# Performance work log

Hardware: AMD Instinct MI355X
Metric: run time of the kernel (lower is better)

## Reference

```python
import jax, jax.numpy as jnp
import numpy as np

N_NODES = 20000
N_EDGES = 320000
N_GRAPHS = 128
IN_CH = 64
DIM = 32
NEG_SLOPE = 0.2
EPS = 1e-16


def _gat_conv(x, src, dst, W, att_src, att_dst, bias, heads, ch):
    """PyG GATConv (concat=True, self-loops already included in src/dst).
    x: [N, F_in]; W: [heads*ch, F_in]; att_*: [heads, ch]; bias: [heads*ch].
    Returns [N, heads*ch]."""
    N = x.shape[0]
    h = (x @ W.T).reshape(N, heads, ch)                      # [N, H, C]
    a_src = (h * att_src[None]).sum(-1)                      # [N, H]
    a_dst = (h * att_dst[None]).sum(-1)                      # [N, H]
    e = jax.nn.leaky_relu(a_src[src] + a_dst[dst], NEG_SLOPE)  # [E, H]
    # segment softmax over edges sharing a destination node
    m = jax.ops.segment_max(e, dst, num_segments=N)          # [N, H]
    ex = jnp.exp(e - m[dst])
    s = jax.ops.segment_sum(ex, dst, num_segments=N)
    alpha = ex / (s[dst] + EPS)                              # [E, H]
    msg = alpha[:, :, None] * h[src]                         # [E, H, C]
    out = jax.ops.segment_sum(msg, dst, num_segments=N)      # [N, H, C]
    return out.reshape(N, heads * ch) + bias[None, :]


def setup_inputs() -> dict:
    key = jax.random.key(0)
    ks = jax.random.split(key, 20)

    x = jax.random.normal(ks[0], (N_NODES, IN_CH), dtype=jnp.float32)
    edge_index = jax.random.randint(ks[1], (2, N_EDGES), 0, N_NODES, dtype=jnp.int64)
    batch = jnp.sort(jax.random.randint(ks[2], (N_NODES,), 0, N_GRAPHS, dtype=jnp.int64))

    def lin_init(k, shape, fan_in):
        return jax.random.normal(k, shape, dtype=jnp.float32) * (1.0 / np.sqrt(fan_in))

    H1, C1 = 5, DIM * 2      # conv1: in -> dim*2, heads 5 -> out dim*10
    H2, C2 = 5, DIM * 3      # conv2: dim*10 -> dim*3, heads 5 -> out dim*15
    H3, C3 = 1, DIM          # conv3: dim*15 -> dim, heads 1

    inp = {
        "x": x,
        "W1": lin_init(ks[3], (H1 * C1, IN_CH), IN_CH),
        "att_src1": lin_init(ks[4], (H1, C1), C1),
        "att_dst1": lin_init(ks[5], (H1, C1), C1),
        "b1": jnp.zeros((H1 * C1,), jnp.float32),
        "W2": lin_init(ks[6], (H2 * C2, H1 * C1), H1 * C1),
        "att_src2": lin_init(ks[7], (H2, C2), C2),
        "att_dst2": lin_init(ks[8], (H2, C2), C2),
        "b2": jnp.zeros((H2 * C2,), jnp.float32),
        "W3": lin_init(ks[9], (H3 * C3, H2 * C2), H2 * C2),
        "att_src3": lin_init(ks[10], (H3, C3), C3),
        "att_dst3": lin_init(ks[11], (H3, C3), C3),
        "b3": jnp.zeros((H3 * C3,), jnp.float32),
        "lin_w": lin_init(ks[12], (1024, DIM), DIM),
        "lin_b": jnp.zeros((1024,), jnp.float32),
        "lin2_w": lin_init(ks[13], (1, 1024), 1024),
        "lin2_b": jnp.zeros((1,), jnp.float32),
        "edge_index": edge_index,
        "batch": batch,
    }
    return inp


def reference(x, W1, att_src1, att_dst1, b1,
              W2, att_src2, att_dst2, b2,
              W3, att_src3, att_dst3, b3,
              lin_w, lin_b, lin2_w, lin2_b,
              edge_index, batch):
    N = x.shape[0]
    # PyG GATConv adds self-loops by default
    loops = jnp.arange(N, dtype=edge_index.dtype)
    src = jnp.concatenate([edge_index[0], loops])
    dst = jnp.concatenate([edge_index[1], loops])

    h = _gat_conv(x, src, dst, W1, att_src1, att_dst1, b1, 5, DIM * 2)
    h = jax.nn.relu(h)                                   # dropout p=0 -> identity
    h = _gat_conv(h, src, dst, W2, att_src2, att_dst2, b2, 5, DIM * 3)
    h = jax.nn.relu(h)
    h = _gat_conv(h, src, dst, W3, att_src3, att_dst3, b3, 1, DIM)
    h = jax.nn.relu(h)

    g = jax.ops.segment_sum(h, batch, num_segments=N_GRAPHS)   # global_add_pool [G, dim]
    g = jax.nn.relu(g @ lin_w.T + lin_b[None, :])
    g = g @ lin2_w.T + lin2_b[None, :]
    return jax.nn.sigmoid(g)                                   # [G, out_channels]
```

## Files before the change

kernel.cpp:

```cpp
#include <hip/hip_runtime.h>
#include <math.h>

#define NN 20000
#define NE 320000
#define NG 128

typedef short short8 __attribute__((ext_vector_type(8)));
typedef float f32x4 __attribute__((ext_vector_type(4)));
typedef float f32x2 __attribute__((ext_vector_type(2)));
typedef unsigned short ushort;
typedef unsigned short ushort4v __attribute__((ext_vector_type(4)));
typedef float float4v __attribute__((ext_vector_type(4)));
typedef unsigned int uint;
typedef unsigned int uint2v __attribute__((ext_vector_type(2)));

__device__ __forceinline__ float b2f(ushort u) {
    unsigned int v = ((unsigned int)u) << 16;
    return __uint_as_float(v);
}
__device__ __forceinline__ ushort f2b(float f) {
    unsigned int u = __float_as_uint(f);
    u = (u + 0x7fff + ((u >> 16) & 1)) >> 16;
    return (ushort)u;
}
__device__ __forceinline__ float lrelu(float x) { return x >= 0.f ? x : 0.2f * x; }
__device__ __forceinline__ unsigned char f2f8(float v) {
    return (unsigned char)(__builtin_amdgcn_cvt_pk_fp8_f32(v, v, 0, false) & 0xff);
}
__device__ __forceinline__ void dec8(uint2v r, f32x2 d[4]) {
    d[0] = __builtin_amdgcn_cvt_pk_f32_fp8(r.x, false);
    d[1] = __builtin_amdgcn_cvt_pk_f32_fp8(r.x, true);
    d[2] = __builtin_amdgcn_cvt_pk_f32_fp8(r.y, false);
    d[3] = __builtin_amdgcn_cvt_pk_f32_fp8(r.y, true);
}

#define CVT_N0 (NN * 64 / 4)
#define CVT_N1 (320 * 64 / 4)
#define CVT_N2 (480 * 320 / 4)
#define CVT_N3 (32 * 480 / 4)
__global__ void f2b4_kernel(const float* __restrict__ a0, ushort* __restrict__ o0,
                            const float* __restrict__ a1, ushort* __restrict__ o1,
                            const float* __restrict__ a2, ushort* __restrict__ o2,
                            const float* __restrict__ a3, ushort* __restrict__ o3) {
    int i = blockIdx.x * blockDim.x + threadIdx.x;
    const float* src; ushort* dst; int li;
    if (i < CVT_N0) { src = a0; dst = o0; li = i; }
    else if (i < CVT_N0 + CVT_N1) { src = a1; dst = o1; li = i - CVT_N0; }
    else if (i < CVT_N0 + CVT_N1 + CVT_N2) { src = a2; dst = o2; li = i - CVT_N0 - CVT_N1; }
    else if (i < CVT_N0 + CVT_N1 + CVT_N2 + CVT_N3) { src = a3; dst = o3; li = i - CVT_N0 - CVT_N1 - CVT_N2; }
    else return;
    float4v v = *(const float4v*)(src + (size_t)li * 4);
    ushort4v r;
    r.x = f2b(v.x); r.y = f2b(v.y); r.z = f2b(v.z); r.w = f2b(v.w);
    *(ushort4v*)(dst + (size_t)li * 4) = r;
}

__global__ void count_kernel(const int* __restrict__ dst, int* __restrict__ cnt, int E) {
    int i = blockIdx.x * blockDim.x + threadIdx.x;
    if (i < E) atomicAdd(&cnt[dst[i]], 1);
}

__global__ __launch_bounds__(1024) void scan_kernel(const int* __restrict__ cnt,
                                                    int* __restrict__ row_start, int n) {
    __shared__ int sh[1024];
    int tid = threadIdx.x;
    int base = tid * 20;
    int local[20];
    int s = 0;
    #pragma unroll
    for (int k = 0; k < 20; ++k) {
        int idx = base + k;
        int v = (idx < n) ? cnt[idx] : 0;
        local[k] = s;
        s += v;
    }
    sh[tid] = s;
    __syncthreads();
    for (int off = 1; off < 1024; off <<= 1) {
        int t = (tid >= off) ? sh[tid - off] : 0;
        __syncthreads();
        sh[tid] += t;
        __syncthreads();
    }
    int pre = (tid == 0) ? 0 : sh[tid - 1];
    #pragma unroll
    for (int k = 0; k < 20; ++k) {
        int idx = base + k;
        if (idx < n) row_start[idx] = pre + local[k];
    }
    if (tid == 1023) row_start[n] = sh[1023];
}

__global__ void fill_kernel(const int* __restrict__ src, const int* __restrict__ dst,
                            const int* __restrict__ row_start, int* __restrict__ cursor,
                            int* __restrict__ csr_src, int E) {
    int i = blockIdx.x * blockDim.x + threadIdx.x;
    if (i < E) {
        int d = dst[i];
        int pos = atomicAdd(&cursor[d], 1);
        csr_src[row_start[d] + pos] = src[i];
    }
}

template <int K, int NF, int H, bool F8>
__global__ __launch_bounds__(256) void gemm_lds(const ushort* __restrict__ A,
                                                const ushort* __restrict__ B,
                                                ushort* __restrict__ C,
                                                unsigned char* __restrict__ C8,
                                                const float* __restrict__ att_src,
                                                const float* __restrict__ att_dst,
                                                float* __restrict__ a_src,
                                                float* __restrict__ a_dst,
                                                int M, int N, int gridx) {
    constexpr int BN = NF * 16;
    constexpr int KC = (K % 160 == 0) ? 160 : K;
    constexpr int NCHK = K / KC;
    constexpr int KS = KC / 32;
    __shared__ ushort Bs[BN][KC + 8];

    const int nwg = gridDim.x;
    int bid = blockIdx.x;
    {
        int q = nwg >> 3, r = nwg & 7;
        int xcd = bid & 7, idx = bid >> 3;
        bid = (xcd < r ? xcd * (q + 1) : r * (q + 1) + (xcd - r) * q) + idx;
    }
    const int by = bid / gridx;
    const int bx = bid % gridx;
    const int bn = bx * BN;

    const int tid = threadIdx.x;
    const int w = tid >> 6;
    const int lane = tid & 63;
    const int l15 = lane & 15;
    const int lhi = lane >> 4;

    const int bm = by * 64 + w * 16;
    int arow = bm + l15;
    if (arow >= M) arow = M - 1;
    const ushort* ap = A + (size_t)arow * K + lhi * 8;

    f32x4 acc[NF];
    #pragma unroll
    for (int f = 0; f < NF; ++f) acc[f] = (f32x4){0.f, 0.f, 0.f, 0.f};

    #pragma unroll
    for (int ch = 0; ch < NCHK; ++ch) {
        const int c0 = ch * KC;
        if (ch > 0) __syncthreads();
        constexpr int NCH = BN * (KC / 8);
        for (int i = tid; i < NCH; i += 256) {
            int r = i / (KC / 8), c8 = i % (KC / 8);
            short8 v = *(const short8*)(B + (size_t)(bn + r) * K + c0 + c8 * 8);
            *(short8*)(&Bs[r][c8 * 8]) = v;
        }
        __syncthreads();

        short8 a_cur = *(const short8*)(ap + c0);
        short8 b_cur[NF], b_nxt[NF];
        #pragma unroll
        for (int f = 0; f < NF; ++f)
            b_cur[f] = *(const short8*)(&Bs[f * 16 + l15][lhi * 8]);

        #pragma unroll
        for (int ks = 0; ks < KS; ++ks) {
            short8 a_nxt = a_cur;
            if (ks + 1 < KS) {
                a_nxt = *(const short8*)(ap + c0 + (ks + 1) * 32);
                #pragma unroll
                for (int f = 0; f < NF; ++f)
                    b_nxt[f] = *(const short8*)(&Bs[f * 16 + l15][(ks + 1) * 32 + lhi * 8]);
            }
            #pragma unroll
            for (int f = 0; f < NF; ++f)
                acc[f] = __builtin_amdgcn_mfma_f32_16x16x32_bf16(a_cur, b_cur[f], acc[f], 0, 0, 0);
            a_cur = a_nxt;
            #pragma unroll
            for (int f = 0; f < NF; ++f) b_cur[f] = b_nxt[f];
        }
    }

    #pragma unroll
    for (int f = 0; f < NF; ++f) {
        #pragma unroll
        for (int j = 0; j < 4; ++j) {
            int row = bm + lhi * 4 + j;
            if (row < M) {
                if (F8) C8[(size_t)row * N + bn + f * 16 + l15] = f2f8(acc[f][j]);
                else    C[(size_t)row * N + bn + f * 16 + l15] = f2b(acc[f][j]);
            }
        }
    }

    float as_v[NF], ad_v[NF];
    #pragma unroll
    for (int f = 0; f < NF; ++f) {
        as_v[f] = att_src[bx * BN + f * 16 + l15];
        ad_v[f] = att_dst[bx * BN + f * 16 + l15];
    }
    #pragma unroll
    for (int j = 0; j < 4; ++j) {
        float ps = 0.f, pd = 0.f;
        #pragma unroll
        for (int f = 0; f < NF; ++f) {
            ps += acc[f][j] * as_v[f];
            pd += acc[f][j] * ad_v[f];
        }
        #pragma unroll
        for (int off = 1; off < 16; off <<= 1) {
            ps += __shfl_xor(ps, off);
            pd += __shfl_xor(pd, off);
        }
        int row = bm + lhi * 4 + j;
        if (l15 == 0 && row < M) {
            a_src[row * H + bx] = ps;
            a_dst[row * H + bx] = pd;
        }
    }
}

template <int H, int C>
__global__ void gat_agg_f8(const unsigned char* __restrict__ h8,
                           const float* __restrict__ a_src, const float* __restrict__ a_dst,
                           const int* __restrict__ row_start, const int* __restrict__ csr_src,
                           const float* __restrict__ bias, ushort* __restrict__ out, int N) {
    constexpr int W = H * C;
    constexpr int VL = W / 8;
    int n = (blockIdx.x * blockDim.x + threadIdx.x) >> 6;
    int lane = threadIdx.x & 63;
    if (n >= N) return;
    bool act = lane < VL;
    int l = act ? lane : 0;
    int hd = (8 * l) / C;
    float adst = a_dst[n * H + hd];

    float m = lrelu(a_src[n * H + hd] + adst);
    float ssum = 1.f;
    f32x2 acc2[4];
    {
        uint2v r = *(const uint2v*)(h8 + (size_t)n * W + 8 * l);
        dec8(r, acc2);
    }

    int rs = row_start[n], re = row_start[n + 1];
    int i = rs;
    for (; i + 8 <= re; i += 8) {
        int s[8]; uint2v r[8]; float e[8];
        #pragma unroll
        for (int j = 0; j < 8; ++j) s[j] = csr_src[i + j];
        #pragma unroll
        for (int j = 0; j < 8; ++j) r[j] = *(const uint2v*)(h8 + (size_t)s[j] * W + 8 * l);
        #pragma unroll
        for (int j = 0; j < 8; ++j) e[j] = lrelu(a_src[s[j] * H + hd] + adst);
        float nm = m;
        #pragma unroll
        for (int j = 0; j < 8; ++j) nm = fmaxf(nm, e[j]);
        float scale = __expf(m - nm);
        m = nm;
        f32x2 sc = {scale, scale};
        #pragma unroll
        for (int d = 0; d < 4; ++d) acc2[d] *= sc;
        ssum *= scale;
        float wsum = 0.f;
        #pragma unroll
        for (int j = 0; j < 8; ++j) {
            float wj = __expf(e[j] - nm);
            wsum += wj;
            f32x2 dd[4];
            dec8(r[j], dd);
            f32x2 vw = {wj, wj};
            #pragma unroll
            for (int d = 0; d < 4; ++d) acc2[d] += vw * dd[d];
        }
        ssum += wsum;
    }
    for (; i + 4 <= re; i += 4) {
        int s[4]; uint2v r[4]; float e[4];
        #pragma unroll
        for (int j = 0; j < 4; ++j) s[j] = csr_src[i + j];
        #pragma unroll
        for (int j = 0; j < 4; ++j) r[j] = *(const uint2v*)(h8 + (size_t)s[j] * W + 8 * l);
        #pragma unroll
        for (int j = 0; j < 4; ++j) e[j] = lrelu(a_src[s[j] * H + hd] + adst);
        float nm = m;
        #pragma unroll
        for (int j = 0; j < 4; ++j) nm = fmaxf(nm, e[j]);
        float scale = __expf(m - nm);
        m = nm;
        f32x2 sc = {scale, scale};
        #pragma unroll
        for (int d = 0; d < 4; ++d) acc2[d] *= sc;
        ssum *= scale;
        float wsum = 0.f;
        #pragma unroll
        for (int j = 0; j < 4; ++j) {
            float wj = __expf(e[j] - nm);
            wsum += wj;
            f32x2 dd[4];
            dec8(r[j], dd);
            f32x2 vw = {wj, wj};
            #pragma unroll
            for (int d = 0; d < 4; ++d) acc2[d] += vw * dd[d];
        }
        ssum += wsum;
    }
    for (; i < re; ++i) {
        int s = csr_src[i];
        uint2v r = *(const uint2v*)(h8 + (size_t)s * W + 8 * l);
        float e = lrelu(a_src[s * H + hd] + adst);
        float nm = fmaxf(m, e);
        float scale = __expf(m - nm);
        m = nm;
        float wgt = __expf(e - nm);
        ssum = ssum * scale + wgt;
        f32x2 dd[4];
        dec8(r, dd);
        f32x2 sc = {scale, scale};
        f32x2 vw = {wgt, wgt};
        #pragma unroll
        for (int d = 0; d < 4; ++d) acc2[d] = acc2[d] * sc + vw * dd[d];
    }

    float inv = 1.f / (ssum + 1e-16f);
    if (act) {
        short8 o;
        #pragma unroll
        for (int d = 0; d < 4; ++d) {
            #pragma unroll
            for (int e2 = 0; e2 < 2; ++e2) {
                float v = acc2[d][e2] * inv + bias[8 * l + 2 * d + e2];
                o[2 * d + e2] = (short)f2b(v > 0.f ? v : 0.f);
            }
        }
        *(short8*)(out + (size_t)n * W + 8 * l) = o;
    }
}

__global__ void gat_agg_c32(const ushort* __restrict__ h, const float* __restrict__ a_src,
                            const float* __restrict__ a_dst, const int* __restrict__ row_start,
                            const int* __restrict__ csr_src, const float* __restrict__ bias,
                            ushort* __restrict__ out, int N) {
    int n = (blockIdx.x * blockDim.x + threadIdx.x) >> 6;
    int lane = threadIdx.x & 63;
    if (n >= N) return;
    int g = lane >> 2;
    int q = lane & 3;
    float adst = a_dst[n];
    int rs = row_start[n];
    int total = row_start[n + 1] - rs + 1;

    float m = -1e30f, ssum = 0.f;
    float acc[8];
    #pragma unroll
    for (int j = 0; j < 8; ++j) acc[j] = 0.f;

    for (int k = g; k < total; k += 16) {
        int s = (k == 0) ? n : csr_src[rs + k - 1];
        float e = lrelu(a_src[s] + adst);
        float nm = fmaxf(m, e);
        float scale = __expf(m - nm);
        m = nm;
        float w = __expf(e - nm);
        ssum = ssum * scale + w;
        short8 r = *(const short8*)(h + (size_t)s * 32 + 8 * q);
        #pragma unroll
        for (int j = 0; j < 8; ++j) acc[j] = acc[j] * scale + w * b2f((ushort)r[j]);
    }

    #pragma unroll
    for (int off = 4; off < 64; off <<= 1) {
        float m2 = __shfl_xor(m, off);
        float s2 = __shfl_xor(ssum, off);
        float nm = fmaxf(m, m2);
        float sc1 = __expf(m - nm), sc2 = __expf(m2 - nm);
        ssum = ssum * sc1 + s2 * sc2;
        #pragma unroll
        for (int j = 0; j < 8; ++j) {
            float a2 = __shfl_xor(acc[j], off);
            acc[j] = acc[j] * sc1 + a2 * sc2;
        }
        m = nm;
    }

    if (lane < 4) {
        float inv = 1.f / (ssum + 1e-16f);
        short8 o;
        #pragma unroll
        for (int j = 0; j < 8; ++j) {
            float v = acc[j] * inv + bias[8 * lane + j];
            o[j] = (short)f2b(v > 0.f ? v : 0.f);
        }
        *(short8*)(out + (size_t)n * 32 + 8 * lane) = o;
    }
}

__global__ __launch_bounds__(256) void pool_graph(const ushort* __restrict__ x,
                                                  const int* __restrict__ batch,
                                                  float* __restrict__ g, int N) {
    int gr = blockIdx.x;
    int a = 0, b = N;
    while (a < b) { int mid = (a + b) >> 1; if (batch[mid] < gr) a = mid + 1; else b = mid; }
    int lo = a;
    b = N;
    while (a < b) { int mid = (a + b) >> 1; if (batch[mid] < gr + 1) a = mid + 1; else b = mid; }
    int hi = a;

    int tid = threadIdx.x;
    int c = tid & 31;
    int grp = tid >> 5;
    float s = 0.f;
    for (int n = lo + grp; n < hi; n += 8)
        s += b2f(x[(size_t)n * 32 + c]);
    __shared__ float sh[8][33];
    sh[grp][c] = s;
    __syncthreads();
    if (tid < 32) {
        float t = 0.f;
        #pragma unroll
        for (int k = 0; k < 8; ++k) t += sh[k][c];
        g[gr * 32 + c] = t;
    }
}

__global__ __launch_bounds__(256) void mlp_fused(const float* __restrict__ gpool,
                                                 const float* __restrict__ lin_w,
                                                 const float* __restrict__ lin_b,
                                                 const float* __restrict__ lin2_w,
                                                 const float* __restrict__ lin2_b,
                                                 float* __restrict__ outp) {
    int gr = blockIdx.x;
    int tid = threadIdx.x;
    __shared__ float grow[32];
    __shared__ float red[4];
    if (tid < 8) {
        float4v v = *(const float4v*)(gpool + gr * 32 + tid * 4);
        *(float4v*)(&grow[tid * 4]) = v;
    }
    __syncthreads();
    float partial = 0.f;
    #pragma unroll
    for (int u = 0; u < 4; ++u) {
        int o = tid + u * 256;
        float s = lin_b[o];
        const float* wp = lin_w + (size_t)o * 32;
        #pragma unroll
        for (int k = 0; k < 32; ++k) s += grow[k] * wp[k];
        s = s > 0.f ? s : 0.f;
        partial += s * lin2_w[o];
    }
    #pragma unroll
    for (int off = 32; off; off >>= 1) partial += __shfl_down(partial, off);
    int lane = tid & 63, wv = tid >> 6;
    if (lane == 0) red[wv] = partial;
    __syncthreads();
    if (tid == 0) {
        float t = red[0] + red[1] + red[2] + red[3] + lin2_b[0];
        outp[gr] = 1.f / (1.f + expf(-t));
    }
}

static inline size_t al256(size_t x) { return (x + 255) & ~(size_t)255; }

extern "C" void kernel_launch(void* const* d_in, const int* in_sizes, int n_in,
                              void* d_out, int out_size, void* d_ws, size_t ws_size,
                              hipStream_t stream) {
    const float* x      = (const float*)d_in[0];
    const float* W1     = (const float*)d_in[1];
    const float* as1    = (const float*)d_in[2];
    const float* ad1    = (const float*)d_in[3];
    const float* b1     = (const float*)d_in[4];
    const float* W2     = (const float*)d_in[5];
    const float* as2    = (const float*)d_in[6];
    const float* ad2    = (const float*)d_in[7];
    const float* b2     = (const float*)d_in[8];
    const float* W3     = (const float*)d_in[9];
    const float* as3    = (const float*)d_in[10];
    const float* ad3    = (const float*)d_in[11];
    const float* b3     = (const float*)d_in[12];
    const float* lin_w  = (const float*)d_in[13];
    const float* lin_b  = (const float*)d_in[14];
    const float* lin2_w = (const float*)d_in[15];
    const float* lin2_b = (const float*)d_in[16];
    const int*   ei     = (const int*)d_in[17];
    const int*   batch  = (const int*)d_in[18];
    float* outp = (float*)d_out;

    const int E = in_sizes[17] / 2;
    const int* e_src = ei;
    const int* e_dst = ei + E;

    char* p = (char*)d_ws;
    ushort* h_bf   = (ushort*)p; p += al256((size_t)NN * 480 * 2);
    ushort* o_bf   = (ushort*)p; p += al256((size_t)NN * 480 * 2);
    unsigned char* h_f8 = (unsigned char*)p; p += al256((size_t)NN * 480);
    ushort* x_bf   = (ushort*)p; p += al256((size_t)NN * 64 * 2);
    ushort* w1_bf  = (ushort*)p; p += al256((size_t)320 * 64 * 2);
    ushort* w2_bf  = (ushort*)p; p += al256((size_t)480 * 320 * 2);
    ushort* w3_bf  = (ushort*)p; p += al256((size_t)32 * 480 * 2);
    float* asrc    = (float*)p; p += al256((size_t)NN * 5 * 4);
    float* adst    = (float*)p; p += al256((size_t)NN * 5 * 4);
    int*   row_st  = (int*)p;   p += al256((size_t)(NN + 1) * 4);
    int*   cnt     = (int*)p;   p += (size_t)NN * 4;
    int*   cursor  = (int*)p;   p += (size_t)NN * 4;
    p = (char*)al256((size_t)p);
    int*   csr_src = (int*)p;   p += al256((size_t)NE * 4);
    float* gpool   = (float*)p; p += al256((size_t)NG * 32 * 4);
    (void)ws_size; (void)n_in; (void)out_size;

    dim3 blk(256);

    hipMemsetAsync(cnt, 0, (size_t)2 * NN * 4, stream);
    count_kernel<<<(E + 255) / 256, 256, 0, stream>>>(e_dst, cnt, E);
    scan_kernel<<<1, 1024, 0, stream>>>(cnt, row_st, NN);
    fill_kernel<<<(E + 255) / 256, 256, 0, stream>>>(e_src, e_dst, row_st, cursor, csr_src, E);

    {
        int tot = CVT_N0 + CVT_N1 + CVT_N2 + CVT_N3;
        f2b4_kernel<<<(tot + 255) / 256, blk, 0, stream>>>(x, x_bf, W1, w1_bf, W2, w2_bf, W3, w3_bf);
    }

    const int MPAN = (NN + 63) / 64;
    const int NBLK = (NN + 3) / 4;
    {
        gemm_lds<64, 4, 5, true><<<5 * MPAN, blk, 0, stream>>>(x_bf, w1_bf, h_bf, h_f8, as1, ad1, asrc, adst, NN, 320, 5);
        gat_agg_f8<5, 64><<<NBLK, blk, 0, stream>>>(h_f8, asrc, adst, row_st, csr_src, b1, o_bf, NN);
    }
    {
        gemm_lds<320, 6, 5, true><<<5 * MPAN, blk, 0, stream>>>(o_bf, w2_bf, h_bf, h_f8, as2, ad2, asrc, adst, NN, 480, 5);
        gat_agg_f8<5, 96><<<NBLK, blk, 0, stream>>>(h_f8, asrc, adst, row_st, csr_src, b2, o_bf, NN);
    }
    {
        gemm_lds<480, 2, 1, false><<<1 * MPAN, blk, 0, stream>>>(o_bf, w3_bf, h_bf, h_f8, as3, ad3, asrc, adst, NN, 32, 1);
        gat_agg_c32<<<NBLK, blk, 0, stream>>>(h_bf, asrc, adst, row_st, csr_src, b3, o_bf, NN);
    }
    pool_graph<<<NG, blk, 0, stream>>>(o_bf, batch, gpool, NN);
    mlp_fused<<<NG, blk, 0, stream>>>(gpool, lin_w, lin_b, lin2_w, lin2_b, outp);
}
```

Measured before the change: 194.2 us.

## Reorder GAT aggregation to head-major thread mapping and fuse small kernels

The fp8 GAT aggregation now assigns one thread per (head, node, 8-column chunk) in head-major order, with an XCD-aware block remap. Previously a 64-lane wave served each node and idle lanes were masked. The 4-edge unrolled loop is dropped. The count and bf16-conversion kernels are merged into one launch, as are pooling and the MLP, to cut launch overhead. Neighbouring threads now handle different nodes, so within a wave the gathers for a given source row become scattered, and per-head a_src lookups repeat across threads.

```diff
diff --git a/kernel.cpp b/kernel.cpp
--- a/kernel.cpp
+++ b/kernel.cpp
@@ -38,26 +38,24 @@
 #define CVT_N1 (320 * 64 / 4)
 #define CVT_N2 (480 * 320 / 4)
 #define CVT_N3 (32 * 480 / 4)
-__global__ void f2b4_kernel(const float* __restrict__ a0, ushort* __restrict__ o0,
-                            const float* __restrict__ a1, ushort* __restrict__ o1,
-                            const float* __restrict__ a2, ushort* __restrict__ o2,
-                            const float* __restrict__ a3, ushort* __restrict__ o3) {
+#define CVT_TOT (CVT_N0 + CVT_N1 + CVT_N2 + CVT_N3)
+__global__ void cvt_count_kernel(const float* __restrict__ a0, ushort* __restrict__ o0,
+                                 const float* __restrict__ a1, ushort* __restrict__ o1,
+                                 const float* __restrict__ a2, ushort* __restrict__ o2,
+                                 const float* __restrict__ a3, ushort* __restrict__ o3,
+                                 const int* __restrict__ e_dst, int* __restrict__ cnt, int E) {
     int i = blockIdx.x * blockDim.x + threadIdx.x;
+    if (i < E) atomicAdd(&cnt[e_dst[i]], 1);
     const float* src; ushort* dst; int li;
     if (i < CVT_N0) { src = a0; dst = o0; li = i; }
     else if (i < CVT_N0 + CVT_N1) { src = a1; dst = o1; li = i - CVT_N0; }
     else if (i < CVT_N0 + CVT_N1 + CVT_N2) { src = a2; dst = o2; li = i - CVT_N0 - CVT_N1; }
-    else if (i < CVT_N0 + CVT_N1 + CVT_N2 + CVT_N3) { src = a3; dst = o3; li = i - CVT_N0 - CVT_N1 - CVT_N2; }
+    else if (i < CVT_TOT) { src = a3; dst = o3; li = i - CVT_N0 - CVT_N1 - CVT_N2; }
     else return;
     float4v v = *(const float4v*)(src + (size_t)li * 4);
     ushort4v r;
     r.x = f2b(v.x); r.y = f2b(v.y); r.z = f2b(v.z); r.w = f2b(v.w);
     *(ushort4v*)(dst + (size_t)li * 4) = r;
-}
-
-__global__ void count_kernel(const int* __restrict__ dst, int* __restrict__ cnt, int E) {
-    int i = blockIdx.x * blockDim.x + threadIdx.x;
-    if (i < E) atomicAdd(&cnt[dst[i]], 1);
 }
 
 __global__ __launch_bounds__(1024) void scan_kernel(const int* __restrict__ cnt,
@@ -220,25 +218,33 @@
 }
 
 template <int H, int C>
-__global__ void gat_agg_f8(const unsigned char* __restrict__ h8,
-                           const float* __restrict__ a_src, const float* __restrict__ a_dst,
-                           const int* __restrict__ row_start, const int* __restrict__ csr_src,
-                           const float* __restrict__ bias, ushort* __restrict__ out, int N) {
+__global__ void gat_agg_f8_hm(const unsigned char* __restrict__ h8,
+                              const float* __restrict__ a_src, const float* __restrict__ a_dst,
+                              const int* __restrict__ row_start, const int* __restrict__ csr_src,
+                              const float* __restrict__ bias, ushort* __restrict__ out, int N) {
     constexpr int W = H * C;
-    constexpr int VL = W / 8;
-    int n = (blockIdx.x * blockDim.x + threadIdx.x) >> 6;
-    int lane = threadIdx.x & 63;
-    if (n >= N) return;
-    bool act = lane < VL;
-    int l = act ? lane : 0;
-    int hd = (8 * l) / C;
+    constexpr int CH = C / 8;
+    const int nwg = gridDim.x;
+    int bid = blockIdx.x;
+    {
+        int q = nwg >> 3, r = nwg & 7;
+        int xcd = bid & 7, idx = bid >> 3;
+        bid = (xcd < r ? xcd * (q + 1) : r * (q + 1) + (xcd - r) * q) + idx;
+    }
+    int t = bid * 256 + (int)threadIdx.x;
+    int hd = t / (N * CH);
+    if (hd >= H) return;
+    int rem = t - hd * (N * CH);
+    int n = rem / CH;
+    int ck = rem - n * CH;
+    int col = hd * CH + ck;
     float adst = a_dst[n * H + hd];
 
     float m = lrelu(a_src[n * H + hd] + adst);
     float ssum = 1.f;
     f32x2 acc2[4];
     {
-        uint2v r = *(const uint2v*)(h8 + (size_t)n * W + 8 * l);
+        uint2v r = *(const uint2v*)(h8 + (size_t)n * W + 8 * col);
         dec8(r, acc2);
     }
 
@@ -249,7 +255,7 @@
         #pragma unroll
         for (int j = 0; j < 8; ++j) s[j] = csr_src[i + j];
         #pragma unroll
-        for (int j = 0; j < 8; ++j) r[j] = *(const uint2v*)(h8 + (size_t)s[j] * W + 8 * l);
+        for (int j = 0; j < 8; ++j) r[j] = *(const uint2v*)(h8 + (size_t)s[j] * W + 8 * col);
         #pragma unroll
         for (int j = 0; j < 8; ++j) e[j] = lrelu(a_src[s[j] * H + hd] + adst);
         float nm = m;
@@ -274,39 +280,9 @@
         }
         ssum += wsum;
     }
-    for (; i + 4 <= re; i += 4) {
-        int s[4]; uint2v r[4]; float e[4];
-        #pragma unroll
-        for (int j = 0; j < 4; ++j) s[j] = csr_src[i + j];
-        #pragma unroll
-        for (int j = 0; j < 4; ++j) r[j] = *(const uint2v*)(h8 + (size_t)s[j] * W + 8 * l);
-        #pragma unroll
-        for (int j = 0; j < 4; ++j) e[j] = lrelu(a_src[s[j] * H + hd] + adst);
-        float nm = m;
-        #pragma unroll
-        for (int j = 0; j < 4; ++j) nm = fmaxf(nm, e[j]);
-        float scale = __expf(m - nm);
-        m = nm;
-        f32x2 sc = {scale, scale};
-        #pragma unroll
-        for (int d = 0; d < 4; ++d) acc2[d] *= sc;
-        ssum *= scale;
-        float wsum = 0.f;
-        #pragma unroll
-        for (int j = 0; j < 4; ++j) {
-            float wj = __expf(e[j] - nm);
-            wsum += wj;
-            f32x2 dd[4];
-            dec8(r[j], dd);
-            f32x2 vw = {wj, wj};
-            #pragma unroll
-            for (int d = 0; d < 4; ++d) acc2[d] += vw * dd[d];
-        }
-        ssum += wsum;
-    }
     for (; i < re; ++i) {
         int s = csr_src[i];
-        uint2v r = *(const uint2v*)(h8 + (size_t)s * W + 8 * l);
+        uint2v r = *(const uint2v*)(h8 + (size_t)s * W + 8 * col);
         float e = lrelu(a_src[s * H + hd] + adst);
         float nm = fmaxf(m, e);
         float scale = __expf(m - nm);
@@ -322,18 +298,16 @@
     }
 
     float inv = 1.f / (ssum + 1e-16f);
-    if (act) {
-        short8 o;
-        #pragma unroll
-        for (int d = 0; d < 4; ++d) {
-            #pragma unroll
-            for (int e2 = 0; e2 < 2; ++e2) {
-                float v = acc2[d][e2] * inv + bias[8 * l + 2 * d + e2];
-                o[2 * d + e2] = (short)f2b(v > 0.f ? v : 0.f);
-            }
-        }
-        *(short8*)(out + (size_t)n * W + 8 * l) = o;
-    }
+    short8 o;
+    #pragma unroll
+    for (int d = 0; d < 4; ++d) {
+        #pragma unroll
+        for (int e2 = 0; e2 < 2; ++e2) {
+            float v = acc2[d][e2] * inv + bias[8 * col + 2 * d + e2];
+            o[2 * d + e2] = (short)f2b(v > 0.f ? v : 0.f);
+        }
+    }
+    *(short8*)(out + (size_t)n * W + 8 * col) = o;
 }
 
 __global__ void gat_agg_c32(const ushort* __restrict__ h, const float* __restrict__ a_src,
@@ -394,9 +368,13 @@
     }
 }
 
-__global__ __launch_bounds__(256) void pool_graph(const ushort* __restrict__ x,
-                                                  const int* __restrict__ batch,
-                                                  float* __restrict__ g, int N) {
+__global__ __launch_bounds__(256) void pool_mlp(const ushort* __restrict__ x,
+                                                const int* __restrict__ batch,
+                                                const float* __restrict__ lin_w,
+                                                const float* __restrict__ lin_b,
+                                                const float* __restrict__ lin2_w,
+                                                const float* __restrict__ lin2_b,
+                                                float* __restrict__ outp, int N) {
     int gr = blockIdx.x;
     int a = 0, b = N;
     while (a < b) { int mid = (a + b) >> 1; if (batch[mid] < gr) a = mid + 1; else b = mid; }
@@ -412,41 +390,27 @@
     for (int n = lo + grp; n < hi; n += 8)
         s += b2f(x[(size_t)n * 32 + c]);
     __shared__ float sh[8][33];
+    __shared__ float grow[32];
+    __shared__ float red[4];
     sh[grp][c] = s;
     __syncthreads();
     if (tid < 32) {
         float t = 0.f;
         #pragma unroll
-        for (int k = 0; k < 8; ++k) t += sh[k][c];
-        g[gr * 32 + c] = t;
-    }
-}
-
-__global__ __launch_bounds__(256) void mlp_fused(const float* __restrict__ gpool,
-                                                 const float* __restrict__ lin_w,
-                                                 const float* __restrict__ lin_b,
-                                                 const float* __restrict__ lin2_w,
-                                                 const float* __restrict__ lin2_b,
-                                                 float* __restrict__ outp) {
-    int gr = blockIdx.x;
-    int tid = threadIdx.x;
-    __shared__ float grow[32];
-    __shared__ float red[4];
-    if (tid < 8) {
-        float4v v = *(const float4v*)(gpool + gr * 32 + tid * 4);
-        *(float4v*)(&grow[tid * 4]) = v;
+        for (int k = 0; k < 8; ++k) t += sh[k][tid];
+        grow[tid] = t;
     }
     __syncthreads();
     float partial = 0.f;
     #pragma unroll
     for (int u = 0; u < 4; ++u) {
         int o = tid + u * 256;
-        float s = lin_b[o];
+        float s2 = lin_b[o];
         const float* wp = lin_w + (size_t)o * 32;
         #pragma unroll
-        for (int k = 0; k < 32; ++k) s += grow[k] * wp[k];
-        s = s > 0.f ? s : 0.f;
-        partial += s * lin2_w[o];
+        for (int k = 0; k < 32; ++k) s2 += grow[k] * wp[k];
+        s2 = s2 > 0.f ? s2 : 0.f;
+        partial += s2 * lin2_w[o];
     }
     #pragma unroll
     for (int off = 32; off; off >>= 1) partial += __shfl_down(partial, off);
@@ -504,35 +468,34 @@
     int*   cursor  = (int*)p;   p += (size_t)NN * 4;
     p = (char*)al256((size_t)p);
     int*   csr_src = (int*)p;   p += al256((size_t)NE * 4);
-    float* gpool   = (float*)p; p += al256((size_t)NG * 32 * 4);
     (void)ws_size; (void)n_in; (void)out_size;
 
     dim3 blk(256);
 
     hipMemsetAsync(cnt, 0, (size_t)2 * NN * 4, stream);
-    count_kernel<<<(E + 255) / 256, 256, 0, stream>>>(e_dst, cnt, E);
+    {
+        int tot = CVT_TOT > NE ? CVT_TOT : NE;
+        cvt_count_kernel<<<(tot + 255) / 256, blk, 0, stream>>>(
+            x, x_bf, W1, w1_bf, W2, w2_bf, W3, w3_bf, e_dst, cnt, E);
+    }
     scan_kernel<<<1, 1024, 0, stream>>>(cnt, row_st, NN);
     fill_kernel<<<(E + 255) / 256, 256, 0, stream>>>(e_src, e_dst, row_st, cursor, csr_src, E);
 
-    {
-        int tot = CVT_N0 + CVT_N1 + CVT_N2 + CVT_N3;
-        f2b4_kernel<<<(tot + 255) / 256, blk, 0, stream>>>(x, x_bf, W1, w1_bf, W2, w2_bf, W3, w3_bf);
-    }
-
     const int MPAN = (NN + 63) / 64;
     const int NBLK = (NN + 3) / 4;
     {
         gemm_lds<64, 4, 5, true><<<5 * MPAN, blk, 0, stream>>>(x_bf, w1_bf, h_bf, h_f8, as1, ad1, asrc, adst, NN, 320, 5);
-        gat_agg_f8<5, 64><<<NBLK, blk, 0, stream>>>(h_f8, asrc, adst, row_st, csr_src, b1, o_bf, NN);
+        int tthr = 5 * NN * 8;
+        gat_agg_f8_hm<5, 64><<<(tthr + 255) / 256, blk, 0, stream>>>(h_f8, asrc, adst, row_st, csr_src, b1, o_bf, NN);
     }
     {
         gemm_lds<320, 6, 5, true><<<5 * MPAN, blk, 0, stream>>>(o_bf, w2_bf, h_bf, h_f8, as2, ad2, asrc, adst, NN, 480, 5);
-        gat_agg_f8<5, 96><<<NBLK, blk, 0, stream>>>(h_f8, asrc, adst, row_st, csr_src, b2, o_bf, NN);
+        int tthr = 5 * NN * 12;
+        gat_agg_f8_hm<5, 96><<<(tthr + 255) / 256, blk, 0, stream>>>(h_f8, asrc, adst, row_st, csr_src, b2, o_bf, NN);
     }
     {
         gemm_lds<480, 2, 1, false><<<1 * MPAN, blk, 0, stream>>>(o_bf, w3_bf, h_bf, h_f8, as3, ad3, asrc, adst, NN, 32, 1);
         gat_agg_c32<<<NBLK, blk, 0, stream>>>(h_bf, asrc, adst, row_st, csr_src, b3, o_bf, NN);
     }
-    pool_graph<<<NG, blk, 0, stream>>>(o_bf, batch, gpool, NN);
-    mlp_fused<<<NG, blk, 0, stream>>>(gpool, lin_w, lin_b, lin2_w, lin2_b, outp);
-}
+    pool_mlp<<<NG, blk, 0, stream>>>(o_bf, batch, lin_w, lin_b, lin2_w, lin2_b, outp, NN);
+}
```

New measurement: 205.0 us. 1.06x slower.
